# Kernel tuning notes

Measured on AMD Instinct MI355X. Metric: run time of the kernel, lower is better.

## Reference

```python
import jax, jax.numpy as jnp
import numpy as np

NUM_STEPS = 100
ALPHA = 0.9      # learn_alpha=False default in snn.Synaptic
THRESHOLD = 1.0
SLOPE = 25.0     # fast_sigmoid default slope

@jax.custom_vjp
def spike_fn(x):
    # Heaviside forward with fast-sigmoid surrogate gradient
    return (x > 0).astype(x.dtype)

def _spike_fwd(x):
    return (x > 0).astype(x.dtype), x

def _spike_bwd(x, g):
    return (g / (SLOPE * jnp.abs(x) + 1.0) ** 2,)

spike_fn.defvjp(_spike_fwd, _spike_bwd)


def setup_inputs() -> dict:
    key = jax.random.key(0)
    k0, k1, k2 = jax.random.split(key, 3)
    B, NI, NH, NO = 4096, 256, 2048, 128
    x = jax.random.normal(k0, (B, NI), dtype=jnp.float32)
    # Linear init scale ~ 1/sqrt(fan_in)
    W1 = jax.random.normal(k1, (NH, NI), dtype=jnp.float32) / np.sqrt(NI)
    b1 = jnp.zeros((NH,), dtype=jnp.float32)
    W2 = jax.random.normal(k2, (NO, NH), dtype=jnp.float32) / np.sqrt(NH)
    b2 = jnp.zeros((NO,), dtype=jnp.float32)
    beta = jnp.asarray(0.85, dtype=jnp.float32)  # learnable scalar
    return {"x": x, "W1": W1, "b1": b1, "W2": W2, "b2": b2, "beta": beta}


def reference(x, W1, b1, W2, b2, beta):
    # cur1 = fc1(x) is identical every step -> hoist (same math)
    cur1 = x @ W1.T + b1                      # [B, NH]
    beta_c = jnp.clip(beta, 0.0, 1.0)
    B, NH = cur1.shape
    z = jnp.zeros((B, NH), dtype=cur1.dtype)

    def step(carry, _):
        syn, mem, _spk = carry
        # reset-by-subtraction from detached pre-update membrane
        reset = jax.lax.stop_gradient((mem > THRESHOLD).astype(mem.dtype))
        syn = ALPHA * syn + cur1
        mem = beta_c * mem + syn - reset * THRESHOLD
        spk = spike_fn(mem - THRESHOLD)
        return (syn, mem, spk), None

    (syn, mem, spk), _ = jax.lax.scan(step, (z, z, z), None, length=NUM_STEPS)
    cur2 = spk @ W2.T + b2                    # [B, NO]
    return cur2
```

## Files before the change

### kernel.cpp

```cpp
#include <hip/hip_runtime.h>
#include <stdint.h>


#define NSTEPS 100

static __device__ __forceinline__ float bf2f(uint16_t b) {
  union { uint32_t u; float f; } v; v.u = ((uint32_t)b) << 16; return v.f;
}

__global__ __launch_bounds__(256, 4) void snn_k1(
    const float* __restrict__ X, const float* __restrict__ W1,
    const float* __restrict__ b1, const float* __restrict__ betap,
    uint16_t* __restrict__ spk)
{
  __shared__ __align__(16) float As[32 * 68];
  __shared__ __align__(16) float Bs[32 * 68];
  const int tid = threadIdx.x;
  const int bm  = blockIdx.y * 64;
  const int bn  = blockIdx.x * 64;
  const int ty  = tid >> 4;
  const int tx  = tid & 15;
  const int sc  = tid & 7;
  const int sr  = tid >> 3;

  float acc[4][4] = {};

  float4 xa[2], wa[2];
  #pragma unroll
  for (int h = 0; h < 2; ++h) {
    const int r = sr + h * 32;
    xa[h] = *(const float4*)(X  + (size_t)(bm + r) * 256 + sc * 4);
    wa[h] = *(const float4*)(W1 + (size_t)(bn + r) * 256 + sc * 4);
  }

  #pragma unroll 1
  for (int k0 = 0; k0 < 256; k0 += 32) {
    #pragma unroll
    for (int h = 0; h < 2; ++h) {
      const int r = sr + h * 32;
      As[(sc * 4 + 0) * 68 + r] = xa[h].x;
      As[(sc * 4 + 1) * 68 + r] = xa[h].y;
      As[(sc * 4 + 2) * 68 + r] = xa[h].z;
      As[(sc * 4 + 3) * 68 + r] = xa[h].w;
      Bs[(sc * 4 + 0) * 68 + r] = wa[h].x;
      Bs[(sc * 4 + 1) * 68 + r] = wa[h].y;
      Bs[(sc * 4 + 2) * 68 + r] = wa[h].z;
      Bs[(sc * 4 + 3) * 68 + r] = wa[h].w;
    }
    __syncthreads();

    if (k0 < 224) {
      const int kn = k0 + 32;
      #pragma unroll
      for (int h = 0; h < 2; ++h) {
        const int r = sr + h * 32;
        xa[h] = *(const float4*)(X  + (size_t)(bm + r) * 256 + kn + sc * 4);
        wa[h] = *(const float4*)(W1 + (size_t)(bn + r) * 256 + kn + sc * 4);
      }
    }

    #pragma unroll
    for (int kk = 0; kk < 32; ++kk) {
      const float4 a4 = *(const float4*)(As + kk * 68 + ty * 4);
      const float4 b4 = *(const float4*)(Bs + kk * 68 + tx * 4);
      const float av[4] = {a4.x, a4.y, a4.z, a4.w};
      const float bv[4] = {b4.x, b4.y, b4.z, b4.w};
      #pragma unroll
      for (int i = 0; i < 4; ++i)
        #pragma unroll
        for (int j = 0; j < 4; ++j)
          acc[i][j] += av[i] * bv[j];
    }
    __syncthreads();
  }

  float beta = betap[0];
  beta = fminf(fmaxf(beta, 0.0f), 1.0f);
  float bias[4];
  #pragma unroll
  for (int j = 0; j < 4; ++j) bias[j] = b1[bn + tx * 4 + j];

  float cc[16];
  #pragma unroll
  for (int i = 0; i < 4; ++i)
    #pragma unroll
    for (int j = 0; j < 4; ++j)
      cc[i * 4 + j] = acc[i][j] + bias[j];

  #pragma unroll
  for (int h = 0; h < 2; ++h) {
    float syn[8], mem[8];
    #pragma unroll
    for (int e = 0; e < 8; ++e) { syn[e] = 0.0f; mem[e] = 0.0f; }

    #pragma unroll 1
    for (int t = 0; t < NSTEPS; ++t) {
      #pragma unroll
      for (int e = 0; e < 8; ++e) {
        const float rst = (mem[e] > 1.0f) ? 1.0f : 0.0f;
        syn[e] = __fadd_rn(__fmul_rn(0.9f, syn[e]), cc[h * 8 + e]);
        mem[e] = __fsub_rn(__fadd_rn(__fmul_rn(beta, mem[e]), syn[e]), rst);
      }
    }

    #pragma unroll
    for (int i = 0; i < 2; ++i) {
      ushort4 o;
      o.x = (mem[i * 4 + 0] > 1.0f) ? (uint16_t)0x3F80u : (uint16_t)0u;
      o.y = (mem[i * 4 + 1] > 1.0f) ? (uint16_t)0x3F80u : (uint16_t)0u;
      o.z = (mem[i * 4 + 2] > 1.0f) ? (uint16_t)0x3F80u : (uint16_t)0u;
      o.w = (mem[i * 4 + 3] > 1.0f) ? (uint16_t)0x3F80u : (uint16_t)0u;
      *(ushort4*)(spk + (size_t)(bm + ty * 4 + h * 2 + i) * 2048 + bn + tx * 4) = o;
    }
  }
}

__global__ __launch_bounds__(256) void snn_k2(
    const uint16_t* __restrict__ spk, const float* __restrict__ W2,
    float* __restrict__ part)
{
  __shared__ __align__(16) float Ss[32 * 20];
  __shared__ __align__(16) float Ws[32 * 132];
  const int tid = threadIdx.x;
  const int bm  = blockIdx.x * 16;
  const int kc  = blockIdx.y;
  const int ty  = tid >> 5;
  const int tx  = tid & 31;
  const int sr  = (tid >> 3) & 15;
  const int sc  = tid & 7;

  float acc[2][4] = {};

  int k0 = kc * 256;
  ushort4 ps;
  if (tid < 128)
    ps = *(const ushort4*)(spk + (size_t)(bm + sr) * 2048 + k0 + sc * 4);
  float4 pw[4];
  #pragma unroll
  for (int it = 0; it < 4; ++it) {
    const int u = it * 256 + tid;
    pw[it] = *(const float4*)(W2 + (size_t)(u >> 3) * 2048 + k0 + (u & 7) * 4);
  }

  #pragma unroll 1
  for (int tile = 0; tile < 8; ++tile) {
    if (tid < 128) {
      Ss[(sc * 4 + 0) * 20 + sr] = bf2f(ps.x);
      Ss[(sc * 4 + 1) * 20 + sr] = bf2f(ps.y);
      Ss[(sc * 4 + 2) * 20 + sr] = bf2f(ps.z);
      Ss[(sc * 4 + 3) * 20 + sr] = bf2f(ps.w);
    }
    #pragma unroll
    for (int it = 0; it < 4; ++it) {
      const int u = it * 256 + tid;
      const int n = u >> 3, c = u & 7;
      Ws[(c * 4 + 0) * 132 + n] = pw[it].x;
      Ws[(c * 4 + 1) * 132 + n] = pw[it].y;
      Ws[(c * 4 + 2) * 132 + n] = pw[it].z;
      Ws[(c * 4 + 3) * 132 + n] = pw[it].w;
    }
    __syncthreads();

    if (tile < 7) {
      const int kn = k0 + 32;
      if (tid < 128)
        ps = *(const ushort4*)(spk + (size_t)(bm + sr) * 2048 + kn + sc * 4);
      #pragma unroll
      for (int it = 0; it < 4; ++it) {
        const int u = it * 256 + tid;
        pw[it] = *(const float4*)(W2 + (size_t)(u >> 3) * 2048 + kn + (u & 7) * 4);
      }
      k0 = kn;
    }

    #pragma unroll
    for (int kk = 0; kk < 32; ++kk) {
      const float2 s2 = *(const float2*)(Ss + kk * 20 + ty * 2);
      const float4 w4 = *(const float4*)(Ws + kk * 132 + tx * 4);
      acc[0][0] += s2.x * w4.x;  acc[0][1] += s2.x * w4.y;
      acc[0][2] += s2.x * w4.z;  acc[0][3] += s2.x * w4.w;
      acc[1][0] += s2.y * w4.x;  acc[1][1] += s2.y * w4.y;
      acc[1][2] += s2.y * w4.z;  acc[1][3] += s2.y * w4.w;
    }
    __syncthreads();
  }

  #pragma unroll
  for (int i = 0; i < 2; ++i) {
    float4 o;
    o.x = acc[i][0]; o.y = acc[i][1]; o.z = acc[i][2]; o.w = acc[i][3];
    *(float4*)(part + ((size_t)kc * 4096 + bm + ty * 2 + i) * 128 + tx * 4) = o;
  }
}

__global__ __launch_bounds__(256) void snn_k3(
    const float* __restrict__ part, const float* __restrict__ b2,
    float* __restrict__ out)
{
  const int idx = blockIdx.x * 256 + threadIdx.x;
  const int m = idx >> 5;
  const int c = (idx & 31) << 2;
  float s0 = 0.f, s1 = 0.f, s2 = 0.f, s3 = 0.f;
  #pragma unroll
  for (int kc = 0; kc < 8; ++kc) {
    const float4 p = *(const float4*)(part + ((size_t)kc * 4096 + m) * 128 + c);
    s0 += p.x; s1 += p.y; s2 += p.z; s3 += p.w;
  }
  float4 o;
  o.x = s0 + b2[c + 0];
  o.y = s1 + b2[c + 1];
  o.z = s2 + b2[c + 2];
  o.w = s3 + b2[c + 3];
  *(float4*)(out + (size_t)m * 128 + c) = o;
}

extern "C" void kernel_launch(void* const* d_in, const int* in_sizes, int n_in,
                              void* d_out, int out_size, void* d_ws, size_t ws_size,
                              hipStream_t stream) {
  const float* X    = (const float*)d_in[0];
  const float* W1   = (const float*)d_in[1];
  const float* b1   = (const float*)d_in[2];
  const float* W2   = (const float*)d_in[3];
  const float* b2   = (const float*)d_in[4];
  const float* beta = (const float*)d_in[5];
  float* out = (float*)d_out;

  uint16_t* spk = (uint16_t*)d_ws;
  float* part = (float*)((char*)d_ws + (size_t)4096 * 2048 * 2);

  snn_k1<<<dim3(32, 64), 256, 0, stream>>>(X, W1, b1, beta, spk);
  snn_k2<<<dim3(256, 8), 256, 0, stream>>>(spk, W2, part);
  snn_k3<<<512, 256, 0, stream>>>(part, b2, out);
}
```

Before: 257.5 us.

## Rewrite second GEMM with bf16 MFMA and larger 128x128 tiles

Result: faster. 215.0 us (-16.5%).

```diff
diff --git a/kernel.cpp b/kernel.cpp
--- a/kernel.cpp
+++ b/kernel.cpp
@@ -2,10 +2,16 @@
 #include <stdint.h>
 
 
+typedef __attribute__((ext_vector_type(8))) short short8;
+typedef __attribute__((ext_vector_type(4))) float floatx4;
+
 #define NSTEPS 100
 
-static __device__ __forceinline__ float bf2f(uint16_t b) {
-  union { uint32_t u; float f; } v; v.u = ((uint32_t)b) << 16; return v.f;
+static __device__ __forceinline__ uint32_t f2bf2(float lo, float hi) {
+  union { float f; uint32_t u; } a, b; a.f = lo; b.f = hi;
+  uint32_t x = (a.u + 0x7FFFu + ((a.u >> 16) & 1u)) >> 16;
+  uint32_t y = (b.u + 0x7FFFu + ((b.u >> 16) & 1u)) & 0xFFFF0000u;
+  return x | y;
 }
 
 __global__ __launch_bounds__(256, 4) void snn_k1(
@@ -115,82 +121,83 @@
   }
 }
 
+#define PS 72
+
 __global__ __launch_bounds__(256) void snn_k2(
     const uint16_t* __restrict__ spk, const float* __restrict__ W2,
     float* __restrict__ part)
 {
-  __shared__ __align__(16) float Ss[32 * 20];
-  __shared__ __align__(16) float Ws[32 * 132];
-  const int tid = threadIdx.x;
-  const int bm  = blockIdx.x * 16;
-  const int kc  = blockIdx.y;
-  const int ty  = tid >> 5;
-  const int tx  = tid & 31;
-  const int sr  = (tid >> 3) & 15;
-  const int sc  = tid & 7;
-
-  float acc[2][4] = {};
-
-  int k0 = kc * 256;
-  ushort4 ps;
-  if (tid < 128)
-    ps = *(const ushort4*)(spk + (size_t)(bm + sr) * 2048 + k0 + sc * 4);
-  float4 pw[4];
-  #pragma unroll
-  for (int it = 0; it < 4; ++it) {
-    const int u = it * 256 + tid;
-    pw[it] = *(const float4*)(W2 + (size_t)(u >> 3) * 2048 + k0 + (u & 7) * 4);
-  }
+  __shared__ short As[128 * PS];
+  __shared__ short Bs[128 * PS];
+  const int tid  = threadIdx.x;
+  const int lane = tid & 63;
+  const int w    = tid >> 6;
+  const int wm   = (w >> 1) * 64;
+  const int wn   = (w & 1) * 64;
+  const int bm   = blockIdx.x * 128;
+  const int kc   = blockIdx.y;
+
+  floatx4 acc[4][4] = {};
 
   #pragma unroll 1
-  for (int tile = 0; tile < 8; ++tile) {
-    if (tid < 128) {
-      Ss[(sc * 4 + 0) * 20 + sr] = bf2f(ps.x);
-      Ss[(sc * 4 + 1) * 20 + sr] = bf2f(ps.y);
-      Ss[(sc * 4 + 2) * 20 + sr] = bf2f(ps.z);
-      Ss[(sc * 4 + 3) * 20 + sr] = bf2f(ps.w);
-    }
-    #pragma unroll
-    for (int it = 0; it < 4; ++it) {
-      const int u = it * 256 + tid;
+  for (int kk = 0; kk < 4; ++kk) {
+    const int k0 = kc * 256 + kk * 64;
+    #pragma unroll
+    for (int p = 0; p < 4; ++p) {
+      const int u = p * 256 + tid;
+      const int r = u >> 3, c = u & 7;
+      const int4 va = *(const int4*)(spk + (size_t)(bm + r) * 2048 + k0 + c * 8);
+      *(int4*)(As + r * PS + c * 8) = va;
+    }
+    #pragma unroll
+    for (int p = 0; p < 4; ++p) {
+      const int u = p * 256 + tid;
       const int n = u >> 3, c = u & 7;
-      Ws[(c * 4 + 0) * 132 + n] = pw[it].x;
-      Ws[(c * 4 + 1) * 132 + n] = pw[it].y;
-      Ws[(c * 4 + 2) * 132 + n] = pw[it].z;
-      Ws[(c * 4 + 3) * 132 + n] = pw[it].w;
-    }
-    __syncthreads();
-
-    if (tile < 7) {
-      const int kn = k0 + 32;
-      if (tid < 128)
-        ps = *(const ushort4*)(spk + (size_t)(bm + sr) * 2048 + kn + sc * 4);
-      #pragma unroll
-      for (int it = 0; it < 4; ++it) {
-        const int u = it * 256 + tid;
-        pw[it] = *(const float4*)(W2 + (size_t)(u >> 3) * 2048 + kn + (u & 7) * 4);
+      const float* wp = W2 + (size_t)n * 2048 + k0 + c * 8;
+      const float4 w0 = *(const float4*)(wp);
+      const float4 w1 = *(const float4*)(wp + 4);
+      int4 pk;
+      pk.x = (int)f2bf2(w0.x, w0.y);
+      pk.y = (int)f2bf2(w0.z, w0.w);
+      pk.z = (int)f2bf2(w1.x, w1.y);
+      pk.w = (int)f2bf2(w1.z, w1.w);
+      *(int4*)(Bs + n * PS + c * 8) = pk;
+    }
+    __syncthreads();
+
+    #pragma unroll
+    for (int ks = 0; ks < 2; ++ks) {
+      const int kb = ks * 4 + (lane >> 4);
+      const int fe = lane & 15;
+      short8 a8[4], b8[4];
+      #pragma unroll
+      for (int tm = 0; tm < 4; ++tm)
+        a8[tm] = *(const short8*)(As + (wm + tm * 16 + fe) * PS + kb * 8);
+      #pragma unroll
+      for (int tn = 0; tn < 4; ++tn)
+        b8[tn] = *(const short8*)(Bs + (wn + tn * 16 + fe) * PS + kb * 8);
+      #pragma unroll
+      for (int tm = 0; tm < 4; ++tm)
+        #pragma unroll
+        for (int tn = 0; tn < 4; ++tn)
+          acc[tm][tn] = __builtin_amdgcn_mfma_f32_16x16x32_bf16(
+              a8[tm], b8[tn], acc[tm][tn], 0, 0, 0);
+    }
+    __syncthreads();
+  }
+
+  const int fe = lane & 15;
+  const int fr = (lane >> 4) * 4;
+  #pragma unroll
+  for (int tm = 0; tm < 4; ++tm)
+    #pragma unroll
+    for (int tn = 0; tn < 4; ++tn)
+      #pragma unroll
+      for (int r = 0; r < 4; ++r) {
+        const int row = bm + wm + tm * 16 + fr + r;
+        const int col = wn + tn * 16 + fe;
+        part[((size_t)kc * 4096 + row) * 128 + col] = acc[tm][tn][r];
       }
-      k0 = kn;
-    }
-
-    #pragma unroll
-    for (int kk = 0; kk < 32; ++kk) {
-      const float2 s2 = *(const float2*)(Ss + kk * 20 + ty * 2);
-      const float4 w4 = *(const float4*)(Ws + kk * 132 + tx * 4);
-      acc[0][0] += s2.x * w4.x;  acc[0][1] += s2.x * w4.y;
-      acc[0][2] += s2.x * w4.z;  acc[0][3] += s2.x * w4.w;
-      acc[1][0] += s2.y * w4.x;  acc[1][1] += s2.y * w4.y;
-      acc[1][2] += s2.y * w4.z;  acc[1][3] += s2.y * w4.w;
-    }
-    __syncthreads();
-  }
-
-  #pragma unroll
-  for (int i = 0; i < 2; ++i) {
-    float4 o;
-    o.x = acc[i][0]; o.y = acc[i][1]; o.z = acc[i][2]; o.w = acc[i][3];
-    *(float4*)(part + ((size_t)kc * 4096 + bm + ty * 2 + i) * 128 + tx * 4) = o;
-  }
 }
 
 __global__ __launch_bounds__(256) void snn_k3(
@@ -229,6 +236,6 @@
   float* part = (float*)((char*)d_ws + (size_t)4096 * 2048 * 2);
 
   snn_k1<<<dim3(32, 64), 256, 0, stream>>>(X, W1, b1, beta, spk);
-  snn_k2<<<dim3(256, 8), 256, 0, stream>>>(spk, W2, part);
+  snn_k2<<<dim3(32, 8), 256, 0, stream>>>(spk, W2, part);
   snn_k3<<<512, 256, 0, stream>>>(part, b2, out);
 }
```
